# Kernel tuning notes

Hardware: AMD Instinct MI355X
Metric: run time of the kernel (lower is better)

Reference implementation:

```python
import jax, jax.numpy as jnp
import numpy as np

N = 100000      # physical-network nodes
E = 3200000     # directed edges (avg degree 32)
DIN = 128       # input_dim
DH = 128        # embedding_dim
DOUT = 128      # output_dim
NUM_GRAPHS = 1


def setup_inputs() -> dict:
    key = jax.random.key(0)
    ks = jax.random.split(key, 8)
    s = 0.05
    x = jax.random.normal(ks[0], (N, DIN), dtype=jnp.float32)
    edge_index = jax.random.randint(ks[1], (2, E), 0, N, dtype=jnp.int64)
    W1 = jax.random.normal(ks[2], (DIN, DH), dtype=jnp.float32) * s
    b1 = jnp.zeros((DH,), dtype=jnp.float32)
    W2 = jax.random.normal(ks[3], (DH, DH), dtype=jnp.float32) * s
    b2 = jnp.zeros((DH,), dtype=jnp.float32)
    W3 = jax.random.normal(ks[4], (DH, DOUT), dtype=jnp.float32) * s
    b3 = jnp.zeros((DOUT,), dtype=jnp.float32)
    return {"x": x, "edge_index": edge_index,
            "W1": W1, "b1": b1, "W2": W2, "b2": b2, "W3": W3, "b3": b3}


def _gcn_norm(edge_index, n_nodes):
    # PyG GCNConv default: add self-loops, symmetric D^{-1/2} (A+I) D^{-1/2} norm.
    loops = jnp.arange(n_nodes, dtype=edge_index.dtype)
    src = jnp.concatenate([edge_index[0], loops])   # [E+N]
    dst = jnp.concatenate([edge_index[1], loops])   # [E+N]
    deg = jax.ops.segment_sum(jnp.ones_like(dst, dtype=jnp.float32), dst,
                              num_segments=n_nodes)
    dinv = jax.lax.rsqrt(deg)  # deg >= 1 because of self-loops
    norm = dinv[src] * dinv[dst]                    # [E+N]
    return src, dst, norm


def _gcn_conv(h, W, b, src, dst, norm, n_nodes):
    h = h @ W                                       # [N, dout] linear first (PyG order)
    msg = h[src] * norm[:, None]                    # gather + edge scaling
    agg = jax.ops.segment_sum(msg, dst, num_segments=n_nodes)  # scatter-add
    return agg + b


def reference(x, edge_index, W1, b1, W2, b2, W3, b3):
    src, dst, norm = _gcn_norm(edge_index, N)
    h = jax.nn.relu(_gcn_conv(x, W1, b1, src, dst, norm, N))
    # dropout is identity in eval mode
    h = jax.nn.relu(_gcn_conv(h, W2, b2, src, dst, norm, N))
    h = _gcn_conv(h, W3, b3, src, dst, norm, N)
    return h.reshape(NUM_GRAPHS, N // NUM_GRAPHS, -1)
```

## Files before the change

### kernel.cpp

```cpp
#include <hip/hip_runtime.h>
#include <cstddef>
#include <cstdint>

#define NN 100000
#define NE 3200000
#define D  128
#define NB 782
#define BSH 7
#define NPB 512
#define CHUNK 6250
#define BCAP 4608

typedef short v8s __attribute__((ext_vector_type(8)));
typedef float v4f __attribute__((ext_vector_type(4)));


__device__ __forceinline__ unsigned short f2bf(float f) {
  uint32_t u = __float_as_uint(f);
  uint32_t r = u + 0x7fff + ((u >> 16) & 1);
  return (unsigned short)(r >> 16);
}
__device__ __forceinline__ float bf_lo(uint32_t v) {
  return __uint_as_float(v << 16);
}
__device__ __forceinline__ float bf_hi(uint32_t v) {
  return __uint_as_float(v & 0xffff0000u);
}


__global__ void k_zero(int* __restrict__ p, int n) {
  int i = blockIdx.x * 256 + threadIdx.x;
  if (i < n) p[i] = 0;
}

__global__ __launch_bounds__(256) void kb_part2(const int* __restrict__ src,
                                                const int* __restrict__ dst,
                                                int* __restrict__ gcur,
                                                uint32_t* __restrict__ ebuf) {
  __shared__ int h[NB];
  __shared__ int cur[NB];
  for (int i = threadIdx.x; i < NB; i += 256) h[i] = 0;
  __syncthreads();
  int lo = blockIdx.x * CHUNK, hi = lo + CHUNK;
  if (hi > NE) hi = NE;
  for (int e = lo + threadIdx.x; e < hi; e += 256)
    atomicAdd(&h[dst[e] >> BSH], 1);
  __syncthreads();
  for (int i = threadIdx.x; i < NB; i += 256)
    cur[i] = h[i] ? atomicAdd(&gcur[i], h[i]) : 0;
  __syncthreads();
  for (int e = lo + threadIdx.x; e < hi; e += 256) {
    int s = src[e], d = dst[e];
    int b = d >> BSH;
    int p = atomicAdd(&cur[b], 1);
    if (p < BCAP)
      ebuf[(size_t)b * BCAP + p] = ((uint32_t)s << BSH) | (uint32_t)(d & 127);
  }
}

__global__ __launch_bounds__(256) void kb_build(const uint32_t* __restrict__ ebuf,
                                                const int* __restrict__ gcur,
                                                int* __restrict__ row_off,
                                                int* __restrict__ row_end,
                                                float* __restrict__ dinv,
                                                int* __restrict__ col) {
  int b = blockIdx.x;
  __shared__ int h[128];
  __shared__ int s[128];
  __shared__ int cur[128];
  if (threadIdx.x < 128) h[threadIdx.x] = 0;
  __syncthreads();
  const uint32_t* eb = ebuf + (size_t)b * BCAP;
  int cnt = gcur[b];
  for (int e = threadIdx.x; e < cnt; e += 256)
    atomicAdd(&h[eb[e] & 127], 1);
  __syncthreads();
  int v = (threadIdx.x < 128) ? h[threadIdx.x] : 0;
  if (threadIdx.x < 128) s[threadIdx.x] = v;
  __syncthreads();
  for (int d = 1; d < 128; d <<= 1) {
    int t = (threadIdx.x < 128 && threadIdx.x >= d) ? s[threadIdx.x - d] : 0;
    __syncthreads();
    if (threadIdx.x < 128) s[threadIdx.x] += t;
    __syncthreads();
  }
  if (threadIdx.x < 128) {
    int ro = b * BCAP + s[threadIdx.x] - v;
    cur[threadIdx.x] = ro;
    int node = b * 128 + threadIdx.x;
    if (node < NN) {
      row_off[node] = ro;
      row_end[node] = ro + v;
      dinv[node] = rsqrtf((float)(v + 1));
    }
  }
  __syncthreads();
  for (int e = threadIdx.x; e < cnt; e += 256) {
    uint32_t p = eb[e];
    int pos = atomicAdd(&cur[p & 127], 1);
    col[pos] = (int)(p >> BSH);
  }
}


__global__ void k_wt3(const float* __restrict__ W1, const float* __restrict__ W2,
                      const float* __restrict__ W3, unsigned short* __restrict__ wt) {
  int idx = blockIdx.x * 256 + threadIdx.x;
  if (idx >= 3 * 16384) return;
  int m = idx >> 14, rem = idx & 16383;
  int k = rem >> 7, c = rem & 127;
  const float* W = (m == 0) ? W1 : (m == 1) ? W2 : W3;
  wt[m * 16384 + c * 128 + k] = f2bf(W[rem]);
}


template <int F32IN>
__global__ __launch_bounds__(256) void k_gemm2(const void* __restrict__ Av,
                                               const unsigned short* __restrict__ wt,
                                               const float* __restrict__ dinv,
                                               unsigned short* __restrict__ C) {
  const int wave = threadIdx.x >> 6;
  const int lane = threadIdx.x & 63;
  const int row0 = blockIdx.x * 256 + wave * 64;
  const int rl = lane & 15;
  const int kg = lane >> 4;

  v4f acc[4][8];
#pragma unroll
  for (int t = 0; t < 4; ++t)
#pragma unroll
    for (int ct = 0; ct < 8; ++ct) acc[t][ct] = (v4f){0.f, 0.f, 0.f, 0.f};

  union U { uint4 u; v8s v; unsigned short us[8]; };

#pragma unroll
  for (int ks = 0; ks < 4; ++ks) {
    U a[4];
#pragma unroll
    for (int t = 0; t < 4; ++t) {
      int r = row0 + t * 16 + rl;
      if (r >= NN) r = NN - 1;
      if (F32IN) {
        const float* ap = (const float*)Av + (size_t)r * D + ks * 32 + kg * 8;
        float4 l4 = *(const float4*)ap;
        float4 h4 = *(const float4*)(ap + 4);
        a[t].us[0] = f2bf(l4.x); a[t].us[1] = f2bf(l4.y);
        a[t].us[2] = f2bf(l4.z); a[t].us[3] = f2bf(l4.w);
        a[t].us[4] = f2bf(h4.x); a[t].us[5] = f2bf(h4.y);
        a[t].us[6] = f2bf(h4.z); a[t].us[7] = f2bf(h4.w);
      } else {
        a[t].u = *(const uint4*)((const unsigned short*)Av +
                                 (size_t)r * D + ks * 32 + kg * 8);
      }
    }
#pragma unroll
    for (int ct = 0; ct < 8; ++ct) {
      U b;
      b.u = *(const uint4*)(wt + (size_t)(ct * 16 + rl) * 128 + ks * 32 + kg * 8);
#pragma unroll
      for (int t = 0; t < 4; ++t)
        acc[t][ct] =
            __builtin_amdgcn_mfma_f32_16x16x32_bf16(a[t].v, b.v, acc[t][ct], 0, 0, 0);
    }
  }

#pragma unroll
  for (int t = 0; t < 4; ++t) {
#pragma unroll
    for (int i = 0; i < 4; ++i) {
      int row = row0 + t * 16 + kg * 4 + i;
      if (row < NN) {
        float dv = dinv[row];
#pragma unroll
        for (int ct = 0; ct < 8; ++ct)
          C[(size_t)row * D + ct * 16 + rl] = f2bf(dv * acc[t][ct][i]);
      }
    }
  }
}


#define AGG8(e0, q0, q1)                                     \
  {                                                          \
    int s0 = col[e0], s1 = col[e0 + 1], s2 = col[e0 + 2],    \
        s3 = col[e0 + 3], s4 = col[e0 + 4], s5 = col[e0 + 5],\
        s6 = col[e0 + 6], s7 = col[e0 + 7];                  \
    uint32_t v0 = tu[(size_t)s0 * 64 + lane];                \
    uint32_t v1 = tu[(size_t)s1 * 64 + lane];                \
    uint32_t v2 = tu[(size_t)s2 * 64 + lane];                \
    uint32_t v3 = tu[(size_t)s3 * 64 + lane];                \
    uint32_t v4 = tu[(size_t)s4 * 64 + lane];                \
    uint32_t v5 = tu[(size_t)s5 * 64 + lane];                \
    uint32_t v6 = tu[(size_t)s6 * 64 + lane];                \
    uint32_t v7 = tu[(size_t)s7 * 64 + lane];                \
    q0 += bf_lo(v0); q1 += bf_hi(v0);                        \
    q0 += bf_lo(v1); q1 += bf_hi(v1);                        \
    q0 += bf_lo(v2); q1 += bf_hi(v2);                        \
    q0 += bf_lo(v3); q1 += bf_hi(v3);                        \
    q0 += bf_lo(v4); q1 += bf_hi(v4);                        \
    q0 += bf_lo(v5); q1 += bf_hi(v5);                        \
    q0 += bf_lo(v6); q1 += bf_hi(v6);                        \
    q0 += bf_lo(v7); q1 += bf_hi(v7);                        \
  }

__global__ __launch_bounds__(256) void k_agg2(
    const uint32_t* __restrict__ tu, const int* __restrict__ row_off,
    const int* __restrict__ row_end, const int* __restrict__ col,
    const float* __restrict__ dinv, const float* __restrict__ bias,
    uint32_t* __restrict__ outb, float* __restrict__ outf, int fin) {
  const int wave = threadIdx.x >> 6;
  const int lane = threadIdx.x & 63;
  const int gA = blockIdx.x * 8 + wave * 2;
  const int gB = gA + 1;

  const float diA = dinv[gA], diB = dinv[gB];

  uint32_t svA = tu[(size_t)gA * 64 + lane];
  uint32_t svB = tu[(size_t)gB * 64 + lane];
  float a0 = bf_lo(svA), a1 = bf_hi(svA);
  float b0 = bf_lo(svB), b1 = bf_hi(svB);

  int eA = row_off[gA], endA = row_end[gA];
  int eB = row_off[gB], endB = row_end[gB];

  while (eA + 8 <= endA && eB + 8 <= endB) {
    int sA0 = col[eA],     sA1 = col[eA + 1], sA2 = col[eA + 2], sA3 = col[eA + 3];
    int sA4 = col[eA + 4], sA5 = col[eA + 5], sA6 = col[eA + 6], sA7 = col[eA + 7];
    int sB0 = col[eB],     sB1 = col[eB + 1], sB2 = col[eB + 2], sB3 = col[eB + 3];
    int sB4 = col[eB + 4], sB5 = col[eB + 5], sB6 = col[eB + 6], sB7 = col[eB + 7];
    uint32_t vA0 = tu[(size_t)sA0 * 64 + lane];
    uint32_t vA1 = tu[(size_t)sA1 * 64 + lane];
    uint32_t vA2 = tu[(size_t)sA2 * 64 + lane];
    uint32_t vA3 = tu[(size_t)sA3 * 64 + lane];
    uint32_t vA4 = tu[(size_t)sA4 * 64 + lane];
    uint32_t vA5 = tu[(size_t)sA5 * 64 + lane];
    uint32_t vA6 = tu[(size_t)sA6 * 64 + lane];
    uint32_t vA7 = tu[(size_t)sA7 * 64 + lane];
    uint32_t vB0 = tu[(size_t)sB0 * 64 + lane];
    uint32_t vB1 = tu[(size_t)sB1 * 64 + lane];
    uint32_t vB2 = tu[(size_t)sB2 * 64 + lane];
    uint32_t vB3 = tu[(size_t)sB3 * 64 + lane];
    uint32_t vB4 = tu[(size_t)sB4 * 64 + lane];
    uint32_t vB5 = tu[(size_t)sB5 * 64 + lane];
    uint32_t vB6 = tu[(size_t)sB6 * 64 + lane];
    uint32_t vB7 = tu[(size_t)sB7 * 64 + lane];
    a0 += bf_lo(vA0); a1 += bf_hi(vA0);
    a0 += bf_lo(vA1); a1 += bf_hi(vA1);
    a0 += bf_lo(vA2); a1 += bf_hi(vA2);
    a0 += bf_lo(vA3); a1 += bf_hi(vA3);
    a0 += bf_lo(vA4); a1 += bf_hi(vA4);
    a0 += bf_lo(vA5); a1 += bf_hi(vA5);
    a0 += bf_lo(vA6); a1 += bf_hi(vA6);
    a0 += bf_lo(vA7); a1 += bf_hi(vA7);
    b0 += bf_lo(vB0); b1 += bf_hi(vB0);
    b0 += bf_lo(vB1); b1 += bf_hi(vB1);
    b0 += bf_lo(vB2); b1 += bf_hi(vB2);
    b0 += bf_lo(vB3); b1 += bf_hi(vB3);
    b0 += bf_lo(vB4); b1 += bf_hi(vB4);
    b0 += bf_lo(vB5); b1 += bf_hi(vB5);
    b0 += bf_lo(vB6); b1 += bf_hi(vB6);
    b0 += bf_lo(vB7); b1 += bf_hi(vB7);
    eA += 8; eB += 8;
  }
  for (; eA + 8 <= endA; eA += 8) AGG8(eA, a0, a1);
  for (; eA < endA; ++eA) {
    uint32_t v = tu[(size_t)col[eA] * 64 + lane];
    a0 += bf_lo(v); a1 += bf_hi(v);
  }
  for (; eB + 8 <= endB; eB += 8) AGG8(eB, b0, b1);
  for (; eB < endB; ++eB) {
    uint32_t v = tu[(size_t)col[eB] * 64 + lane];
    b0 += bf_lo(v); b1 += bf_hi(v);
  }

  int c = lane * 2;
  float rA0 = diA * a0 + bias[c];
  float rA1 = diA * a1 + bias[c + 1];
  float rB0 = diB * b0 + bias[c];
  float rB1 = diB * b1 + bias[c + 1];
  if (!fin) {
    rA0 = fmaxf(rA0, 0.f); rA1 = fmaxf(rA1, 0.f);
    rB0 = fmaxf(rB0, 0.f); rB1 = fmaxf(rB1, 0.f);
    outb[(size_t)gA * 64 + lane] = (uint32_t)f2bf(rA0) | ((uint32_t)f2bf(rA1) << 16);
    outb[(size_t)gB * 64 + lane] = (uint32_t)f2bf(rB0) | ((uint32_t)f2bf(rB1) << 16);
  } else {
    *(float2*)(outf + (size_t)gA * D + c) = make_float2(rA0, rA1);
    *(float2*)(outf + (size_t)gB * D + c) = make_float2(rB0, rB1);
  }
}


extern "C" void kernel_launch(void* const* d_in, const int* in_sizes, int n_in,
                              void* d_out, int out_size, void* d_ws, size_t ws_size,
                              hipStream_t stream) {
  const float* x  = (const float*)d_in[0];
  const int*   ei = (const int*)d_in[1];
  const float* W1 = (const float*)d_in[2];
  const float* b1 = (const float*)d_in[3];
  const float* W2 = (const float*)d_in[4];
  const float* b2 = (const float*)d_in[5];
  const float* W3 = (const float*)d_in[6];
  const float* b3 = (const float*)d_in[7];
  float* out = (float*)d_out;

  char* base = (char*)d_ws;
  size_t o = 0;
  auto take = [&](size_t bytes) {
    void* p = base + o;
    o += (bytes + 255) & ~(size_t)255;
    return p;
  };
  int*   row_off = (int*)take((size_t)NN * 4);
  int*   row_end = (int*)take((size_t)NN * 4);
  float* dinv    = (float*)take((size_t)NN * 4);
  int*   gcur    = (int*)take((size_t)NB * 4);
  unsigned short* wt = (unsigned short*)take(3 * 16384 * 2);
  void* region1 = take((size_t)NN * D * 2);
  int*  col     = (int*)take((size_t)NB * BCAP * 4);
  unsigned short* t0 = (unsigned short*)take((size_t)NN * D * 2);

  uint32_t* ebuf = (uint32_t*)region1;
  unsigned short* h = (unsigned short*)region1;

  const int* src = ei;
  const int* dst = ei + NE;

  k_zero  <<<(NB + 255) / 256, 256, 0, stream>>>(gcur, NB);
  kb_part2<<<NPB, 256, 0, stream>>>(src, dst, gcur, ebuf);
  kb_build<<<NB, 256, 0, stream>>>(ebuf, gcur, row_off, row_end, dinv, col);
  k_wt3   <<<192, 256, 0, stream>>>(W1, W2, W3, wt);

  const int gB = (NN + 255) / 256;
  const int aB = NN / 8;

  k_gemm2<1><<<gB, 256, 0, stream>>>(x, wt, dinv, t0);
  k_agg2<<<aB, 256, 0, stream>>>((const uint32_t*)t0, row_off, row_end, col, dinv,
                                 b1, (uint32_t*)h, nullptr, 0);
  k_gemm2<0><<<gB, 256, 0, stream>>>(h, wt + 16384, dinv, t0);
  k_agg2<<<aB, 256, 0, stream>>>((const uint32_t*)t0, row_off, row_end, col, dinv,
                                 b2, (uint32_t*)h, nullptr, 0);
  k_gemm2<0><<<gB, 256, 0, stream>>>(h, wt + 32768, dinv, t0);
  k_agg2<<<aB, 256, 0, stream>>>((const uint32_t*)t0, row_off, row_end, col, dinv,
                                 b3, nullptr, out, 1);
}
```

Before: 489.4 us.

## Fuse aggregation with next layer's GEMM via LDS-staged MFMA epilogue

Replaces the separate bf16 GEMM for layers 2 and 3 with a fused aggregate-then-transform kernel. Each 512-thread block aggregates 16 nodes, writes the activated bf16 rows to swizzled LDS, and multiplies them by the next weight matrix with MFMA, applying the dinv scaling before storing. This removes two GEMM launches and the write and re-read of the intermediate hidden activations. In exchange it adds a block barrier and a small per-block MFMA tile, and it reloads the weight tile from global memory in every block.

```diff
diff --git a/kernel.cpp b/kernel.cpp
--- a/kernel.cpp
+++ b/kernel.cpp
@@ -114,8 +114,7 @@
 }
 
 
-template <int F32IN>
-__global__ __launch_bounds__(256) void k_gemm2(const void* __restrict__ Av,
+__global__ __launch_bounds__(256) void k_gemm2(const float* __restrict__ A,
                                                const unsigned short* __restrict__ wt,
                                                const float* __restrict__ dinv,
                                                unsigned short* __restrict__ C) {
@@ -140,18 +139,13 @@
     for (int t = 0; t < 4; ++t) {
       int r = row0 + t * 16 + rl;
       if (r >= NN) r = NN - 1;
-      if (F32IN) {
-        const float* ap = (const float*)Av + (size_t)r * D + ks * 32 + kg * 8;
-        float4 l4 = *(const float4*)ap;
-        float4 h4 = *(const float4*)(ap + 4);
-        a[t].us[0] = f2bf(l4.x); a[t].us[1] = f2bf(l4.y);
-        a[t].us[2] = f2bf(l4.z); a[t].us[3] = f2bf(l4.w);
-        a[t].us[4] = f2bf(h4.x); a[t].us[5] = f2bf(h4.y);
-        a[t].us[6] = f2bf(h4.z); a[t].us[7] = f2bf(h4.w);
-      } else {
-        a[t].u = *(const uint4*)((const unsigned short*)Av +
-                                 (size_t)r * D + ks * 32 + kg * 8);
-      }
+      const float* ap = A + (size_t)r * D + ks * 32 + kg * 8;
+      float4 l4 = *(const float4*)ap;
+      float4 h4 = *(const float4*)(ap + 4);
+      a[t].us[0] = f2bf(l4.x); a[t].us[1] = f2bf(l4.y);
+      a[t].us[2] = f2bf(l4.z); a[t].us[3] = f2bf(l4.w);
+      a[t].us[4] = f2bf(h4.x); a[t].us[5] = f2bf(h4.y);
+      a[t].us[6] = f2bf(h4.z); a[t].us[7] = f2bf(h4.w);
     }
 #pragma unroll
     for (int ct = 0; ct < 8; ++ct) {
@@ -203,11 +197,120 @@
     q0 += bf_lo(v7); q1 += bf_hi(v7);                        \
   }
 
+#define GATHER_BODY()                                                        \
+  uint32_t svA = tu[(size_t)gA * 64 + lane];                                 \
+  uint32_t svB = tu[(size_t)gB * 64 + lane];                                 \
+  float a0 = bf_lo(svA), a1 = bf_hi(svA);                                    \
+  float b0 = bf_lo(svB), b1 = bf_hi(svB);                                    \
+  int eA = row_off[gA], endA = row_end[gA];                                  \
+  int eB = row_off[gB], endB = row_end[gB];                                  \
+  while (eA + 8 <= endA && eB + 8 <= endB) {                                 \
+    int sA0 = col[eA],     sA1 = col[eA + 1], sA2 = col[eA + 2],             \
+        sA3 = col[eA + 3], sA4 = col[eA + 4], sA5 = col[eA + 5],             \
+        sA6 = col[eA + 6], sA7 = col[eA + 7];                                \
+    int sB0 = col[eB],     sB1 = col[eB + 1], sB2 = col[eB + 2],             \
+        sB3 = col[eB + 3], sB4 = col[eB + 4], sB5 = col[eB + 5],             \
+        sB6 = col[eB + 6], sB7 = col[eB + 7];                                \
+    uint32_t vA0 = tu[(size_t)sA0 * 64 + lane];                              \
+    uint32_t vA1 = tu[(size_t)sA1 * 64 + lane];                              \
+    uint32_t vA2 = tu[(size_t)sA2 * 64 + lane];                              \
+    uint32_t vA3 = tu[(size_t)sA3 * 64 + lane];                              \
+    uint32_t vA4 = tu[(size_t)sA4 * 64 + lane];                              \
+    uint32_t vA5 = tu[(size_t)sA5 * 64 + lane];                              \
+    uint32_t vA6 = tu[(size_t)sA6 * 64 + lane];                              \
+    uint32_t vA7 = tu[(size_t)sA7 * 64 + lane];                              \
+    uint32_t vB0 = tu[(size_t)sB0 * 64 + lane];                              \
+    uint32_t vB1 = tu[(size_t)sB1 * 64 + lane];                              \
+    uint32_t vB2 = tu[(size_t)sB2 * 64 + lane];                              \
+    uint32_t vB3 = tu[(size_t)sB3 * 64 + lane];                              \
+    uint32_t vB4 = tu[(size_t)sB4 * 64 + lane];                              \
+    uint32_t vB5 = tu[(size_t)sB5 * 64 + lane];                              \
+    uint32_t vB6 = tu[(size_t)sB6 * 64 + lane];                              \
+    uint32_t vB7 = tu[(size_t)sB7 * 64 + lane];                              \
+    a0 += bf_lo(vA0); a1 += bf_hi(vA0);                                      \
+    a0 += bf_lo(vA1); a1 += bf_hi(vA1);                                      \
+    a0 += bf_lo(vA2); a1 += bf_hi(vA2);                                      \
+    a0 += bf_lo(vA3); a1 += bf_hi(vA3);                                      \
+    a0 += bf_lo(vA4); a1 += bf_hi(vA4);                                      \
+    a0 += bf_lo(vA5); a1 += bf_hi(vA5);                                      \
+    a0 += bf_lo(vA6); a1 += bf_hi(vA6);                                      \
+    a0 += bf_lo(vA7); a1 += bf_hi(vA7);                                      \
+    b0 += bf_lo(vB0); b1 += bf_hi(vB0);                                      \
+    b0 += bf_lo(vB1); b1 += bf_hi(vB1);                                      \
+    b0 += bf_lo(vB2); b1 += bf_hi(vB2);                                      \
+    b0 += bf_lo(vB3); b1 += bf_hi(vB3);                                      \
+    b0 += bf_lo(vB4); b1 += bf_hi(vB4);                                      \
+    b0 += bf_lo(vB5); b1 += bf_hi(vB5);                                      \
+    b0 += bf_lo(vB6); b1 += bf_hi(vB6);                                      \
+    b0 += bf_lo(vB7); b1 += bf_hi(vB7);                                      \
+    eA += 8; eB += 8;                                                        \
+  }                                                                          \
+  for (; eA + 8 <= endA; eA += 8) AGG8(eA, a0, a1);                          \
+  for (; eA < endA; ++eA) {                                                  \
+    uint32_t v = tu[(size_t)col[eA] * 64 + lane];                            \
+    a0 += bf_lo(v); a1 += bf_hi(v);                                          \
+  }                                                                          \
+  for (; eB + 8 <= endB; eB += 8) AGG8(eB, b0, b1);                          \
+  for (; eB < endB; ++eB) {                                                  \
+    uint32_t v = tu[(size_t)col[eB] * 64 + lane];                            \
+    b0 += bf_lo(v); b1 += bf_hi(v);                                          \
+  }
+
+
+__global__ __launch_bounds__(512) void k_aggf(
+    const uint32_t* __restrict__ tu, const int* __restrict__ row_off,
+    const int* __restrict__ row_end, const int* __restrict__ col,
+    const float* __restrict__ dinv, const float* __restrict__ bias,
+    const unsigned short* __restrict__ wt, unsigned short* __restrict__ t_out) {
+  const int wave = threadIdx.x >> 6;
+  const int lane = threadIdx.x & 63;
+  const int gA = blockIdx.x * 16 + wave * 2;
+  const int gB = gA + 1;
+
+  __shared__ uint32_t lds[16 * 64];
+
+  const float diA = dinv[gA], diB = dinv[gB];
+
+  GATHER_BODY();
+
+  int c = lane * 2;
+  float bl = bias[c], bh = bias[c + 1];
+  float rA0 = fmaxf(diA * a0 + bl, 0.f);
+  float rA1 = fmaxf(diA * a1 + bh, 0.f);
+  float rB0 = fmaxf(diB * b0 + bl, 0.f);
+  float rB1 = fmaxf(diB * b1 + bh, 0.f);
+
+  const int rA = wave * 2, rB = rA + 1;
+  lds[rA * 64 + (lane ^ ((rA & 7) << 2))] =
+      (uint32_t)f2bf(rA0) | ((uint32_t)f2bf(rA1) << 16);
+  lds[rB * 64 + (lane ^ ((rB & 7) << 2))] =
+      (uint32_t)f2bf(rB0) | ((uint32_t)f2bf(rB1) << 16);
+  __syncthreads();
+
+  const int rl = lane & 15;
+  const int kg = lane >> 4;
+  union U { uint4 u; v8s v; };
+  v4f acc = (v4f){0.f, 0.f, 0.f, 0.f};
+#pragma unroll
+  for (int ks = 0; ks < 4; ++ks) {
+    U a, b;
+    a.u = *(const uint4*)&lds[rl * 64 + ((ks * 16 + kg * 4) ^ ((rl & 7) << 2))];
+    b.u = *(const uint4*)(wt + (size_t)(wave * 16 + rl) * 128 + ks * 32 + kg * 8);
+    acc = __builtin_amdgcn_mfma_f32_16x16x32_bf16(a.v, b.v, acc, 0, 0, 0);
+  }
+#pragma unroll
+  for (int i = 0; i < 4; ++i) {
+    int node = blockIdx.x * 16 + kg * 4 + i;
+    t_out[(size_t)node * D + wave * 16 + rl] = f2bf(dinv[node] * acc[i]);
+  }
+}
+
+
 __global__ __launch_bounds__(256) void k_agg2(
     const uint32_t* __restrict__ tu, const int* __restrict__ row_off,
     const int* __restrict__ row_end, const int* __restrict__ col,
     const float* __restrict__ dinv, const float* __restrict__ bias,
-    uint32_t* __restrict__ outb, float* __restrict__ outf, int fin) {
+    float* __restrict__ outf) {
   const int wave = threadIdx.x >> 6;
   const int lane = threadIdx.x & 63;
   const int gA = blockIdx.x * 8 + wave * 2;
@@ -215,78 +318,15 @@
 
   const float diA = dinv[gA], diB = dinv[gB];
 
-  uint32_t svA = tu[(size_t)gA * 64 + lane];
-  uint32_t svB = tu[(size_t)gB * 64 + lane];
-  float a0 = bf_lo(svA), a1 = bf_hi(svA);
-  float b0 = bf_lo(svB), b1 = bf_hi(svB);
-
-  int eA = row_off[gA], endA = row_end[gA];
-  int eB = row_off[gB], endB = row_end[gB];
-
-  while (eA + 8 <= endA && eB + 8 <= endB) {
-    int sA0 = col[eA],     sA1 = col[eA + 1], sA2 = col[eA + 2], sA3 = col[eA + 3];
-    int sA4 = col[eA + 4], sA5 = col[eA + 5], sA6 = col[eA + 6], sA7 = col[eA + 7];
-    int sB0 = col[eB],     sB1 = col[eB + 1], sB2 = col[eB + 2], sB3 = col[eB + 3];
-    int sB4 = col[eB + 4], sB5 = col[eB + 5], sB6 = col[eB + 6], sB7 = col[eB + 7];
-    uint32_t vA0 = tu[(size_t)sA0 * 64 + lane];
-    uint32_t vA1 = tu[(size_t)sA1 * 64 + lane];
-    uint32_t vA2 = tu[(size_t)sA2 * 64 + lane];
-    uint32_t vA3 = tu[(size_t)sA3 * 64 + lane];
-    uint32_t vA4 = tu[(size_t)sA4 * 64 + lane];
-    uint32_t vA5 = tu[(size_t)sA5 * 64 + lane];
-    uint32_t vA6 = tu[(size_t)sA6 * 64 + lane];
-    uint32_t vA7 = tu[(size_t)sA7 * 64 + lane];
-    uint32_t vB0 = tu[(size_t)sB0 * 64 + lane];
-    uint32_t vB1 = tu[(size_t)sB1 * 64 + lane];
-    uint32_t vB2 = tu[(size_t)sB2 * 64 + lane];
-    uint32_t vB3 = tu[(size_t)sB3 * 64 + lane];
-    uint32_t vB4 = tu[(size_t)sB4 * 64 + lane];
-    uint32_t vB5 = tu[(size_t)sB5 * 64 + lane];
-    uint32_t vB6 = tu[(size_t)sB6 * 64 + lane];
-    uint32_t vB7 = tu[(size_t)sB7 * 64 + lane];
-    a0 += bf_lo(vA0); a1 += bf_hi(vA0);
-    a0 += bf_lo(vA1); a1 += bf_hi(vA1);
-    a0 += bf_lo(vA2); a1 += bf_hi(vA2);
-    a0 += bf_lo(vA3); a1 += bf_hi(vA3);
-    a0 += bf_lo(vA4); a1 += bf_hi(vA4);
-    a0 += bf_lo(vA5); a1 += bf_hi(vA5);
-    a0 += bf_lo(vA6); a1 += bf_hi(vA6);
-    a0 += bf_lo(vA7); a1 += bf_hi(vA7);
-    b0 += bf_lo(vB0); b1 += bf_hi(vB0);
-    b0 += bf_lo(vB1); b1 += bf_hi(vB1);
-    b0 += bf_lo(vB2); b1 += bf_hi(vB2);
-    b0 += bf_lo(vB3); b1 += bf_hi(vB3);
-    b0 += bf_lo(vB4); b1 += bf_hi(vB4);
-    b0 += bf_lo(vB5); b1 += bf_hi(vB5);
-    b0 += bf_lo(vB6); b1 += bf_hi(vB6);
-    b0 += bf_lo(vB7); b1 += bf_hi(vB7);
-    eA += 8; eB += 8;
-  }
-  for (; eA + 8 <= endA; eA += 8) AGG8(eA, a0, a1);
-  for (; eA < endA; ++eA) {
-    uint32_t v = tu[(size_t)col[eA] * 64 + lane];
-    a0 += bf_lo(v); a1 += bf_hi(v);
-  }
-  for (; eB + 8 <= endB; eB += 8) AGG8(eB, b0, b1);
-  for (; eB < endB; ++eB) {
-    uint32_t v = tu[(size_t)col[eB] * 64 + lane];
-    b0 += bf_lo(v); b1 += bf_hi(v);
-  }
+  GATHER_BODY();
 
   int c = lane * 2;
   float rA0 = diA * a0 + bias[c];
   float rA1 = diA * a1 + bias[c + 1];
   float rB0 = diB * b0 + bias[c];
   float rB1 = diB * b1 + bias[c + 1];
-  if (!fin) {
-    rA0 = fmaxf(rA0, 0.f); rA1 = fmaxf(rA1, 0.f);
-    rB0 = fmaxf(rB0, 0.f); rB1 = fmaxf(rB1, 0.f);
-    outb[(size_t)gA * 64 + lane] = (uint32_t)f2bf(rA0) | ((uint32_t)f2bf(rA1) << 16);
-    outb[(size_t)gB * 64 + lane] = (uint32_t)f2bf(rB0) | ((uint32_t)f2bf(rB1) << 16);
-  } else {
-    *(float2*)(outf + (size_t)gA * D + c) = make_float2(rA0, rA1);
-    *(float2*)(outf + (size_t)gB * D + c) = make_float2(rB0, rB1);
-  }
+  *(float2*)(outf + (size_t)gA * D + c) = make_float2(rA0, rA1);
+  *(float2*)(outf + (size_t)gB * D + c) = make_float2(rB0, rB1);
 }
 
 
@@ -320,7 +360,7 @@
   unsigned short* t0 = (unsigned short*)take((size_t)NN * D * 2);
 
   uint32_t* ebuf = (uint32_t*)region1;
-  unsigned short* h = (unsigned short*)region1;
+  unsigned short* t1 = (unsigned short*)region1;
 
   const int* src = ei;
   const int* dst = ei + NE;
@@ -331,15 +371,14 @@
   k_wt3   <<<192, 256, 0, stream>>>(W1, W2, W3, wt);
 
   const int gB = (NN + 255) / 256;
+  const int fB = NN / 16;
   const int aB = NN / 8;
 
-  k_gemm2<1><<<gB, 256, 0, stream>>>(x, wt, dinv, t0);
+  k_gemm2<<<gB, 256, 0, stream>>>(x, wt, dinv, t0);
+  k_aggf<<<fB, 512, 0, stream>>>((const uint32_t*)t0, row_off, row_end, col, dinv,
+                                 b1, wt + 16384, t1);
+  k_aggf<<<fB, 512, 0, stream>>>((const uint32_t*)t1, row_off, row_end, col, dinv,
+                                 b2, wt + 32768, t0);
   k_agg2<<<aB, 256, 0, stream>>>((const uint32_t*)t0, row_off, row_end, col, dinv,
-                                 b1, (uint32_t*)h, nullptr, 0);
-  k_gemm2<0><<<gB, 256, 0, stream>>>(h, wt + 16384, dinv, t0);
-  k_agg2<<<aB, 256, 0, stream>>>((const uint32_t*)t0, row_off, row_end, col, dinv,
-                                 b2, (uint32_t*)h, nullptr, 0);
-  k_gemm2<0><<<gB, 256, 0, stream>>>(h, wt + 32768, dinv, t0);
-  k_agg2<<<aB, 256, 0, stream>>>((const uint32_t*)t0, row_off, row_end, col, dinv,
-                                 b3, nullptr, out, 1);
-}
+                                 b3, out);
+}
```

Measured after the change: 486.6 us. About the same (-0.6%).
